# Performance work log

Hardware: AMD Instinct MI355X
Metric: run time of the kernel (lower is better)

Reference implementation:

```python
import jax, jax.numpy as jnp
import numpy as np

B, S, D, H = 2, 2048, 2048, 16
DK = D // H
EPS = 1e-5


def _layernorm(x, g, b):
    m = jnp.mean(x, axis=-1, keepdims=True)
    v = jnp.mean(jnp.square(x - m), axis=-1, keepdims=True)
    return (x - m) * jax.lax.rsqrt(v + EPS) * g + b


def setup_inputs() -> dict:
    key = jax.random.key(0)
    ks = jax.random.split(key, 12)
    w = lambda k, shape: jax.random.normal(k, shape, jnp.float32) * 0.02
    return {
        "src": jax.random.normal(ks[0], (B, S, D), jnp.float32),
        "src_mask": jnp.tril(jnp.ones((S, S), jnp.float32))[None, None],  # [1,1,S,S] causal
        "Wq": w(ks[1], (D, D)), "bq": jnp.zeros((D,), jnp.float32),
        "Wk": w(ks[2], (D, D)), "bk": jnp.zeros((D,), jnp.float32),
        "Wv": w(ks[3], (D, D)), "bv": jnp.zeros((D,), jnp.float32),
        "Wo": w(ks[4], (D, D)), "bo": jnp.zeros((D,), jnp.float32),
        "ln1_g": jnp.ones((D,), jnp.float32), "ln1_b": jnp.zeros((D,), jnp.float32),
        "ln2_g": jnp.ones((D,), jnp.float32), "ln2_b": jnp.zeros((D,), jnp.float32),
        "W1": w(ks[5], (D, 4 * D)), "b1": jnp.zeros((4 * D,), jnp.float32),
        "W2": w(ks[6], (4 * D, D)), "b2": jnp.zeros((D,), jnp.float32),
    }


def reference(src, src_mask, Wq, bq, Wk, bk, Wv, bv, Wo, bo,
              ln1_g, ln1_b, ln2_g, ln2_b, W1, b1, W2, b2):
    b, s, d = src.shape
    dk = d // H
    # --- pre-LN attention ---
    x = _layernorm(src, ln1_g, ln1_b)
    q = (x @ Wq + bq).reshape(b, s, H, dk).transpose(0, 2, 1, 3)  # [b,h,s,dk]
    k = (x @ Wk + bk).reshape(b, s, H, dk).transpose(0, 2, 1, 3)
    v = (x @ Wv + bv).reshape(b, s, H, dk).transpose(0, 2, 1, 3)
    scores = jnp.einsum('bhqd,bhkd->bhqk', q, k) / np.sqrt(dk).astype(np.float32)
    scores = jnp.where(src_mask > 0, scores, jnp.float32(-1e9))
    attn = jax.nn.softmax(scores, axis=-1)
    ctx = jnp.einsum('bhqk,bhkd->bhqd', attn, v)
    ctx = ctx.transpose(0, 2, 1, 3).reshape(b, s, d)
    x = src + (ctx @ Wo + bo)  # residual (dropout is identity at eval)
    # --- pre-LN MLP ---
    y = _layernorm(x, ln2_g, ln2_b)
    y = jax.nn.gelu(y @ W1 + b1, approximate=False) @ W2 + b2
    return x + y
```

## Files before the change

### kernel.cpp

```cpp
#include <hip/hip_runtime.h>
#include <hip/hip_bf16.h>
#include <math.h>

#define DEV __device__ __forceinline__

typedef __attribute__((ext_vector_type(8))) short short8;
typedef __attribute__((ext_vector_type(4))) float f32x4;

DEV short f2bf(float f) {
  union { float f; unsigned u; } v; v.f = f;
  unsigned r = v.u + 0x7fffu + ((v.u >> 16) & 1u);
  return (short)(r >> 16);
}

DEV void gload16(const void* g, void* l) {
  __builtin_amdgcn_global_load_lds(
      (__attribute__((address_space(1))) void*)g,
      (__attribute__((address_space(3))) void*)l, 16, 0, 0);
}

__global__ __launch_bounds__(256) void ln_kernel(
    const float* __restrict__ x, const float* __restrict__ g,
    const float* __restrict__ b, short* __restrict__ out) {
  int row = blockIdx.x;
  const float* xr = x + (size_t)row * 2048;
  int tid = threadIdx.x;
  float4 a0 = ((const float4*)xr)[tid * 2];
  float4 a1 = ((const float4*)xr)[tid * 2 + 1];
  float s = a0.x + a0.y + a0.z + a0.w + a1.x + a1.y + a1.z + a1.w;
  float q = a0.x*a0.x + a0.y*a0.y + a0.z*a0.z + a0.w*a0.w
          + a1.x*a1.x + a1.y*a1.y + a1.z*a1.z + a1.w*a1.w;
#pragma unroll
  for (int off = 32; off; off >>= 1) { s += __shfl_xor(s, off); q += __shfl_xor(q, off); }
  __shared__ float red[8];
  int w = tid >> 6;
  if ((tid & 63) == 0) { red[w] = s; red[4 + w] = q; }
  __syncthreads();
  s = red[0] + red[1] + red[2] + red[3];
  q = red[4] + red[5] + red[6] + red[7];
  float mean = s * (1.0f / 2048.0f);
  float var  = q * (1.0f / 2048.0f) - mean * mean;
  float rstd = rsqrtf(var + 1e-5f);
  float xv[8] = {a0.x, a0.y, a0.z, a0.w, a1.x, a1.y, a1.z, a1.w};
  short8 o;
#pragma unroll
  for (int j = 0; j < 8; ++j) {
    int col = tid * 8 + j;
    o[j] = f2bf((xv[j] - mean) * rstd * g[col] + b[col]);
  }
  *(short8*)(out + (size_t)row * 2048 + tid * 8) = o;
}

__global__ __launch_bounds__(256) void wt_kernel(
    const float* __restrict__ W, short* __restrict__ Wt, int K, int N) {
  __shared__ short tile[64][65];
  int k0 = blockIdx.x * 64, n0 = blockIdx.y * 64;
  int tx = threadIdx.x, ty = threadIdx.y;
#pragma unroll
  for (int r = 0; r < 16; ++r) {
    int kl = ty + r * 4;
    tile[kl][tx] = f2bf(W[(size_t)(k0 + kl) * N + n0 + tx]);
  }
  __syncthreads();
#pragma unroll
  for (int r = 0; r < 16; ++r) {
    int nl = ty + r * 4;
    Wt[(size_t)(n0 + nl) * K + k0 + tx] = tile[tx][nl];
  }
}

template <int EPI>
__global__ __launch_bounds__(256) void gemm_kernel(
    const short* __restrict__ A, const short* __restrict__ Bt, int K, int N,
    const float* __restrict__ bp1, const float* __restrict__ bp2,
    const float* __restrict__ bp3, const float* __restrict__ res,
    short* __restrict__ outb, float* __restrict__ outf, short* __restrict__ vt) {
  __shared__ char As[8192];
  __shared__ char Bs[8192];
  int tid = threadIdx.x, lane = tid & 63, w = tid >> 6;
  int wm = w >> 1, wn = w & 1;
  int hi = lane >> 4, lo = lane & 15;
  int bm = blockIdx.y * 128, bn = blockIdx.x * 128;

  int srow = 2 * w * 16 + (lane >> 2);
  int sslot = lane & 3;
  const short* Ag0 = A  + (size_t)(bm + srow) * K      + (sslot ^ (srow & 3)) * 8;
  const short* Ag1 = A  + (size_t)(bm + srow + 16) * K + (sslot ^ (srow & 3)) * 8;
  const short* Bg0 = Bt + (size_t)(bn + srow) * K      + (sslot ^ (srow & 3)) * 8;
  const short* Bg1 = Bt + (size_t)(bn + srow + 16) * K + (sslot ^ (srow & 3)) * 8;
  char* Al0 = As + 2 * w * 1024;  char* Al1 = Al0 + 1024;
  char* Bl0 = Bs + 2 * w * 1024;  char* Bl1 = Bl0 + 1024;

  const char* aRd[4]; const char* bRd[4];
#pragma unroll
  for (int i = 0; i < 4; ++i) {
    int ra = wm * 64 + i * 16 + lo;
    aRd[i] = As + ra * 64 + ((hi ^ (ra & 3)) << 4);
    int rb = wn * 64 + i * 16 + lo;
    bRd[i] = Bs + rb * 64 + ((hi ^ (rb & 3)) << 4);
  }

  f32x4 acc[4][4] = {};

  for (int k0 = 0; k0 < K; k0 += 32) {
    gload16(Ag0 + k0, Al0);
    gload16(Ag1 + k0, Al1);
    gload16(Bg0 + k0, Bl0);
    gload16(Bg1 + k0, Bl1);
    __syncthreads();
    short8 af[4], bf[4];
#pragma unroll
    for (int i = 0; i < 4; ++i) af[i] = *(const short8*)aRd[i];
#pragma unroll
    for (int i = 0; i < 4; ++i) bf[i] = *(const short8*)bRd[i];
#pragma unroll
    for (int mi = 0; mi < 4; ++mi)
#pragma unroll
      for (int ni = 0; ni < 4; ++ni)
        acc[mi][ni] = __builtin_amdgcn_mfma_f32_16x16x32_bf16(af[mi], bf[ni], acc[mi][ni], 0, 0, 0);
    __syncthreads();
  }

#pragma unroll
  for (int mi = 0; mi < 4; ++mi) {
#pragma unroll
    for (int ni = 0; ni < 4; ++ni) {
      int n = bn + wn * 64 + ni * 16 + lo;
#pragma unroll
      for (int r = 0; r < 4; ++r) {
        int m = bm + wm * 64 + mi * 16 + hi * 4 + r;
        float v = acc[mi][ni][r];
        if (EPI == 0) {
          float bb = (n < 2048) ? bp1[n] : (n < 4096) ? bp2[n - 2048] : bp3[n - 4096];
          v += bb;
          if (n < 2048) v *= 0.08838834764831845f;
          outb[(size_t)m * N + n] = f2bf(v);
          if (n >= 4096) {
            int b_ = m >> 11, s_ = m & 2047, h_ = (n - 4096) >> 7, dk = (n - 4096) & 127;
            vt[((size_t)((b_ * 16 + h_) * 128 + dk) << 11) + s_] = f2bf(v);
          }
        } else if (EPI == 1) {
          outf[(size_t)m * N + n] = res[(size_t)m * N + n] + v + bp1[n];
        } else {
          float t = v + bp1[n];
          outb[(size_t)m * N + n] = f2bf(0.5f * t * (1.0f + erff(t * 0.70710678118654752f)));
        }
      }
    }
  }
}

__global__ __launch_bounds__(256) void attn_kernel(
    const short* __restrict__ qkv, const short* __restrict__ vtb,
    short* __restrict__ ctx) {
  __shared__ char Kl[16384];
  __shared__ char Vl[16384];
  __shared__ char Pl[16384];
  int qt = blockIdx.x, bh = blockIdx.y;
  int b = bh >> 4, h = bh & 15;
  int tid = threadIdx.x, lane = tid & 63, w = tid >> 6;
  int hi = lane >> 4, lo = lane & 15;

  short8 qf[2][4];
#pragma unroll
  for (int mi = 0; mi < 2; ++mi)
#pragma unroll
    for (int ks = 0; ks < 4; ++ks) {
      int row = b * 2048 + qt * 128 + w * 32 + mi * 16 + lo;
      int col = h * 128 + ks * 32 + hi * 8;
      qf[mi][ks] = *(const short8*)(qkv + (size_t)row * 6144 + col);
    }

  f32x4 ao[2][8] = {};
  float mst[2][4], lst[2][4];
#pragma unroll
  for (int i = 0; i < 2; ++i)
#pragma unroll
    for (int r = 0; r < 4; ++r) { mst[i][r] = -1e30f; lst[i][r] = 0.f; }

  int nt = 2 * qt + 2;
  for (int t = 0; t < nt; ++t) {
    __syncthreads();
#pragma unroll
    for (int i = 0; i < 4; ++i) {
      int c = w * 4 + i;
      int kr = c * 4 + (lane >> 4);
      int dk16 = lo ^ (kr & 7);
      const short* kg = qkv + (size_t)(b * 2048 + t * 64 + kr) * 6144
                            + 2048 + h * 128 + dk16 * 8;
      gload16(kg, Kl + c * 1024);
      int vr = c * 8 + (lane >> 3);
      int kv16 = (lane & 7) ^ (vr & 7);
      const short* vg = vtb + (size_t)(bh * 128 + vr) * 2048 + t * 64 + kv16 * 8;
      gload16(vg, Vl + c * 1024);
    }
    __syncthreads();

    f32x4 sc[2][4] = {};
#pragma unroll
    for (int ks = 0; ks < 4; ++ks) {
      short8 kf[4];
#pragma unroll
      for (int ni = 0; ni < 4; ++ni) {
        int r = ni * 16 + lo;
        kf[ni] = *(const short8*)(Kl + r * 256 + (((ks * 4 + hi) ^ (r & 7)) << 4));
      }
#pragma unroll
      for (int mi = 0; mi < 2; ++mi)
#pragma unroll
        for (int ni = 0; ni < 4; ++ni)
          sc[mi][ni] = __builtin_amdgcn_mfma_f32_16x16x32_bf16(qf[mi][ks], kf[ni], sc[mi][ni], 0, 0, 0);
    }

    if (t >= 2 * qt) {
#pragma unroll
      for (int mi = 0; mi < 2; ++mi)
#pragma unroll
        for (int ni = 0; ni < 4; ++ni)
#pragma unroll
          for (int r = 0; r < 4; ++r) {
            int qrow = qt * 128 + w * 32 + mi * 16 + hi * 4 + r;
            int kv = t * 64 + ni * 16 + lo;
            if (kv > qrow) sc[mi][ni][r] = -1e9f;
          }
    }

#pragma unroll
    for (int mi = 0; mi < 2; ++mi)
#pragma unroll
      for (int r = 0; r < 4; ++r) {
        float vm = fmaxf(fmaxf(sc[mi][0][r], sc[mi][1][r]),
                         fmaxf(sc[mi][2][r], sc[mi][3][r]));
#pragma unroll
        for (int off = 8; off; off >>= 1) vm = fmaxf(vm, __shfl_xor(vm, off));
        float mn = fmaxf(mst[mi][r], vm);
        float corr = __expf(mst[mi][r] - mn);
        float ps = 0.f;
#pragma unroll
        for (int ni = 0; ni < 4; ++ni) {
          float p = __expf(sc[mi][ni][r] - mn);
          sc[mi][ni][r] = p; ps += p;
        }
#pragma unroll
        for (int off = 8; off; off >>= 1) ps += __shfl_xor(ps, off);
        lst[mi][r] = lst[mi][r] * corr + ps;
        mst[mi][r] = mn;
#pragma unroll
        for (int ni = 0; ni < 8; ++ni) ao[mi][ni][r] *= corr;
      }

#pragma unroll
    for (int mi = 0; mi < 2; ++mi)
#pragma unroll
      for (int ni = 0; ni < 4; ++ni)
#pragma unroll
        for (int r = 0; r < 4; ++r) {
          int rl = w * 32 + mi * 16 + hi * 4 + r;
          int byte = (rl * 128 + (ni * 16 + lo) * 2) ^ ((rl & 7) << 4);
          *(short*)(Pl + byte) = f2bf(sc[mi][ni][r]);
        }

#pragma unroll
    for (int ks = 0; ks < 2; ++ks) {
      short8 pf[2];
#pragma unroll
      for (int mi = 0; mi < 2; ++mi) {
        int r = w * 32 + mi * 16 + lo;
        pf[mi] = *(const short8*)(Pl + r * 128 + (((ks * 4 + hi) ^ (r & 7)) << 4));
      }
#pragma unroll
      for (int ni = 0; ni < 8; ++ni) {
        int r = ni * 16 + lo;
        short8 vf = *(const short8*)(Vl + r * 128 + (((ks * 4 + hi) ^ (r & 7)) << 4));
#pragma unroll
        for (int mi = 0; mi < 2; ++mi)
          ao[mi][ni] = __builtin_amdgcn_mfma_f32_16x16x32_bf16(pf[mi], vf, ao[mi][ni], 0, 0, 0);
      }
    }
  }

#pragma unroll
  for (int mi = 0; mi < 2; ++mi)
#pragma unroll
    for (int r = 0; r < 4; ++r) {
      float inv = 1.0f / lst[mi][r];
      int m = b * 2048 + qt * 128 + w * 32 + mi * 16 + hi * 4 + r;
#pragma unroll
      for (int ni = 0; ni < 8; ++ni) {
        int col = h * 128 + ni * 16 + lo;
        ctx[(size_t)m * 2048 + col] = f2bf(ao[mi][ni][r] * inv);
      }
    }
}

extern "C" void kernel_launch(void* const* d_in, const int* in_sizes, int n_in,
                              void* d_out, int out_size, void* d_ws, size_t ws_size,
                              hipStream_t stream) {
  const float* src = (const float*)d_in[0];
  const float* Wq = (const float*)d_in[2];  const float* bq = (const float*)d_in[3];
  const float* Wk = (const float*)d_in[4];  const float* bk = (const float*)d_in[5];
  const float* Wv = (const float*)d_in[6];  const float* bv = (const float*)d_in[7];
  const float* Wo = (const float*)d_in[8];  const float* bo = (const float*)d_in[9];
  const float* g1 = (const float*)d_in[10]; const float* be1 = (const float*)d_in[11];
  const float* g2 = (const float*)d_in[12]; const float* be2 = (const float*)d_in[13];
  const float* W1 = (const float*)d_in[14]; const float* b1 = (const float*)d_in[15];
  const float* W2 = (const float*)d_in[16]; const float* b2 = (const float*)d_in[17];

  char* ws = (char*)d_ws;
  short* x_ln = (short*)(ws);
  short* qkvb = (short*)(ws + 16777216);
  short* vtb  = (short*)(ws + 67108864);
  short* ctxb = (short*)(ws + 83886080);
  float* xbuf = (float*)(ws + 100663296);
  short* wt   = (short*)(ws + 134217728);
  short* hb   = (short*)(ws + 16777216);

  dim3 tb(64, 4);

  wt_kernel<<<dim3(32, 32), tb, 0, stream>>>(Wq, wt,                2048, 2048);
  wt_kernel<<<dim3(32, 32), tb, 0, stream>>>(Wk, wt + 2048 * 2048,  2048, 2048);
  wt_kernel<<<dim3(32, 32), tb, 0, stream>>>(Wv, wt + 4096 * 2048,  2048, 2048);
  ln_kernel<<<4096, 256, 0, stream>>>(src, g1, be1, x_ln);
  gemm_kernel<0><<<dim3(48, 32), 256, 0, stream>>>(
      x_ln, wt, 2048, 6144, bq, bk, bv, nullptr, qkvb, nullptr, vtb);
  attn_kernel<<<dim3(16, 32), 256, 0, stream>>>(qkvb, vtb, ctxb);
  wt_kernel<<<dim3(32, 32), tb, 0, stream>>>(Wo, wt, 2048, 2048);
  gemm_kernel<1><<<dim3(16, 32), 256, 0, stream>>>(
      ctxb, wt, 2048, 2048, bo, nullptr, nullptr, src, nullptr, xbuf, nullptr);
  ln_kernel<<<4096, 256, 0, stream>>>(xbuf, g2, be2, x_ln);
  wt_kernel<<<dim3(32, 128), tb, 0, stream>>>(W1, wt, 2048, 8192);
  gemm_kernel<2><<<dim3(64, 32), 256, 0, stream>>>(
      x_ln, wt, 2048, 8192, b1, nullptr, nullptr, nullptr, hb, nullptr, nullptr);
  wt_kernel<<<dim3(128, 32), tb, 0, stream>>>(W2, wt, 8192, 2048);
  gemm_kernel<1><<<dim3(16, 32), 256, 0, stream>>>(
      hb, wt, 8192, 2048, b2, nullptr, nullptr, xbuf, nullptr, (float*)d_out, nullptr);

  (void)in_sizes; (void)n_in; (void)out_size; (void)ws_size;
}
```

Measured before the change: 1.123 ms.

## Replace GEMM with 8-wave multi-buffered pipelined kernel using larger tiles

Replaces the single-buffered 128x128 four-wave GEMM with an eight-wave kernel that uses 256-wide N tiles (and 256 or 128 M tiles). It keeps four LDS stages, prefetches the next K-slices with global_load_lds while MFMAs run, and interleaves fine-grained barriers with setprio. The aim is to hide global memory latency, which the old loop exposed by syncing before every 32-wide K step, and to raise data reuse per block. In exchange it uses much more LDS, hand-written vmcnt waits that must match the load counts, and fewer blocks for the 2048-wide GEMMs.

New measurement: 985.7 us. 1.14x faster.

```diff
diff --git a/kernel.cpp b/kernel.cpp
--- a/kernel.cpp
+++ b/kernel.cpp
@@ -6,6 +6,8 @@
 
 typedef __attribute__((ext_vector_type(8))) short short8;
 typedef __attribute__((ext_vector_type(4))) float f32x4;
+
+template<bool B> struct BoolC { static constexpr bool value = B; };
 
 DEV short f2bf(float f) {
   union { float f; unsigned u; } v; v.f = f;
@@ -17,6 +19,17 @@
   __builtin_amdgcn_global_load_lds(
       (__attribute__((address_space(1))) void*)g,
       (__attribute__((address_space(3))) void*)l, 16, 0, 0);
+}
+
+DEV void bar() {
+  asm volatile("" ::: "memory");
+  __builtin_amdgcn_s_barrier();
+  asm volatile("" ::: "memory");
+}
+template<int N> DEV void vwait() {
+  if constexpr (N == 0)      asm volatile("s_waitcnt vmcnt(0)" ::: "memory");
+  else if constexpr (N == 3) asm volatile("s_waitcnt vmcnt(3)" ::: "memory");
+  else                       asm volatile("s_waitcnt vmcnt(4)" ::: "memory");
 }
 
 __global__ __launch_bounds__(256) void ln_kernel(
@@ -69,67 +82,140 @@
   }
 }
 
-template <int EPI>
-__global__ __launch_bounds__(256) void gemm_kernel(
+template <int BM, int EPI>
+__global__ __launch_bounds__(512, 2) void gemm8_kernel(
     const short* __restrict__ A, const short* __restrict__ Bt, int K, int N,
     const float* __restrict__ bp1, const float* __restrict__ bp2,
     const float* __restrict__ bp3, const float* __restrict__ res,
     short* __restrict__ outb, float* __restrict__ outf, short* __restrict__ vt) {
-  __shared__ char As[8192];
-  __shared__ char Bs[8192];
+  constexpr int MF  = BM / 32;
+  constexpr int MG  = MF / 2;
+  constexpr int SA  = BM * 64;
+  constexpr int SB  = 16384;
+  constexpr int CPA = BM / 128;
+  constexpr int CPB = 2;
+  constexpr int NW  = CPA + CPB;
+  __shared__ char lds[4 * SA + 4 * SB];
+  char* Ab = lds;
+  char* Bb = lds + 4 * SA;
   int tid = threadIdx.x, lane = tid & 63, w = tid >> 6;
-  int wm = w >> 1, wn = w & 1;
-  int hi = lane >> 4, lo = lane & 15;
-  int bm = blockIdx.y * 128, bn = blockIdx.x * 128;
-
-  int srow = 2 * w * 16 + (lane >> 2);
-  int sslot = lane & 3;
-  const short* Ag0 = A  + (size_t)(bm + srow) * K      + (sslot ^ (srow & 3)) * 8;
-  const short* Ag1 = A  + (size_t)(bm + srow + 16) * K + (sslot ^ (srow & 3)) * 8;
-  const short* Bg0 = Bt + (size_t)(bn + srow) * K      + (sslot ^ (srow & 3)) * 8;
-  const short* Bg1 = Bt + (size_t)(bn + srow + 16) * K + (sslot ^ (srow & 3)) * 8;
-  char* Al0 = As + 2 * w * 1024;  char* Al1 = Al0 + 1024;
-  char* Bl0 = Bs + 2 * w * 1024;  char* Bl1 = Bl0 + 1024;
-
-  const char* aRd[4]; const char* bRd[4];
-#pragma unroll
-  for (int i = 0; i < 4; ++i) {
-    int ra = wm * 64 + i * 16 + lo;
-    aRd[i] = As + ra * 64 + ((hi ^ (ra & 3)) << 4);
-    int rb = wn * 64 + i * 16 + lo;
-    bRd[i] = Bs + rb * 64 + ((hi ^ (rb & 3)) << 4);
-  }
-
-  f32x4 acc[4][4] = {};
-
-  for (int k0 = 0; k0 < K; k0 += 32) {
-    gload16(Ag0 + k0, Al0);
-    gload16(Ag1 + k0, Al1);
-    gload16(Bg0 + k0, Bl0);
-    gload16(Bg1 + k0, Bl1);
-    __syncthreads();
-    short8 af[4], bf[4];
-#pragma unroll
-    for (int i = 0; i < 4; ++i) af[i] = *(const short8*)aRd[i];
-#pragma unroll
-    for (int i = 0; i < 4; ++i) bf[i] = *(const short8*)bRd[i];
-#pragma unroll
-    for (int mi = 0; mi < 4; ++mi)
-#pragma unroll
-      for (int ni = 0; ni < 4; ++ni)
-        acc[mi][ni] = __builtin_amdgcn_mfma_f32_16x16x32_bf16(af[mi], bf[ni], acc[mi][ni], 0, 0, 0);
-    __syncthreads();
-  }
-
-#pragma unroll
-  for (int mi = 0; mi < 4; ++mi) {
-#pragma unroll
-    for (int ni = 0; ni < 4; ++ni) {
-      int n = bn + wn * 64 + ni * 16 + lo;
+  int wm = w >> 2, wn = w & 3, hi = lane >> 4, lo = lane & 15;
+  int bm = blockIdx.y * BM, bn = blockIdx.x * 256;
+
+  const char* gA[CPA]; int lA[CPA];
+  const char* gB[CPB]; int lB[CPB];
+#pragma unroll
+  for (int i = 0; i < CPA; ++i) {
+    int c = w * CPA + i, r = c * 16 + (lane >> 2);
+    gA[i] = (const char*)(A + (size_t)(bm + r) * K) + (((lane & 3) ^ ((r >> 1) & 3)) << 4);
+    lA[i] = c * 1024;
+  }
+#pragma unroll
+  for (int i = 0; i < CPB; ++i) {
+    int c = w * CPB + i, r = c * 16 + (lane >> 2);
+    gB[i] = (const char*)(Bt + (size_t)(bn + r) * K) + (((lane & 3) ^ ((r >> 1) & 3)) << 4);
+    lB[i] = c * 1024;
+  }
+  auto stA = [&](int g) {
+    char* d = Ab + (g & 3) * SA;
+#pragma unroll
+    for (int i = 0; i < CPA; ++i) gload16(gA[i] + (size_t)g * 64, d + lA[i]);
+  };
+  auto stB = [&](int g) {
+    char* d = Bb + (g & 3) * SB;
+#pragma unroll
+    for (int i = 0; i < CPB; ++i) gload16(gB[i] + (size_t)g * 64, d + lB[i]);
+  };
+
+  int offA[MF], offB[4];
+#pragma unroll
+  for (int m = 0; m < MF; ++m) {
+    int r = wm * (BM / 2) + m * 16 + lo;
+    offA[m] = r * 64 + ((hi ^ ((r >> 1) & 3)) << 4);
+  }
+#pragma unroll
+  for (int n = 0; n < 4; ++n) {
+    int r = wn * 64 + n * 16 + lo;
+    offB[n] = r * 64 + ((hi ^ ((r >> 1) & 3)) << 4);
+  }
+
+  f32x4 acc[MF][4];
+#pragma unroll
+  for (int m = 0; m < MF; ++m)
+#pragma unroll
+    for (int n = 0; n < 4; ++n) acc[m][n] = (f32x4){0.f, 0.f, 0.f, 0.f};
+
+  stA(0); stB(0); stA(1); stB(1);
+  vwait<NW>(); bar();
+
+  int NT = K >> 6;
+  auto tile = [&](int t, auto stc) {
+    constexpr bool ST = decltype(stc)::value;
+    char* sa0 = Ab + ((2 * t) & 3) * SA;     char* sb0 = Bb + ((2 * t) & 3) * SB;
+    char* sa1 = Ab + ((2 * t + 1) & 3) * SA; char* sb1 = Bb + ((2 * t + 1) & 3) * SB;
+    short8 bf[4], af[MG];
+#pragma unroll
+    for (int n = 0; n < 4; ++n) bf[n] = *(const short8*)(sb0 + offB[n]);
+#pragma unroll
+    for (int m = 0; m < MG; ++m) af[m] = *(const short8*)(sa0 + offA[m]);
+    if constexpr (ST) stA(2 * t + 2);
+    bar(); __builtin_amdgcn_s_setprio(1);
+#pragma unroll
+    for (int m = 0; m < MG; ++m)
+#pragma unroll
+      for (int n = 0; n < 4; ++n)
+        acc[m][n] = __builtin_amdgcn_mfma_f32_16x16x32_bf16(af[m], bf[n], acc[m][n], 0, 0, 0);
+    __builtin_amdgcn_s_setprio(0); bar();
+#pragma unroll
+    for (int m = 0; m < MG; ++m) af[m] = *(const short8*)(sa0 + offA[MG + m]);
+    if constexpr (ST) stB(2 * t + 2);
+    bar(); __builtin_amdgcn_s_setprio(1);
+#pragma unroll
+    for (int m = 0; m < MG; ++m)
+#pragma unroll
+      for (int n = 0; n < 4; ++n)
+        acc[MG + m][n] = __builtin_amdgcn_mfma_f32_16x16x32_bf16(af[m], bf[n], acc[MG + m][n], 0, 0, 0);
+    __builtin_amdgcn_s_setprio(0);
+    if constexpr (ST) vwait<NW>(); else vwait<0>();
+    bar();
+#pragma unroll
+    for (int n = 0; n < 4; ++n) bf[n] = *(const short8*)(sb1 + offB[n]);
+#pragma unroll
+    for (int m = 0; m < MG; ++m) af[m] = *(const short8*)(sa1 + offA[m]);
+    if constexpr (ST) stA(2 * t + 3);
+    bar(); __builtin_amdgcn_s_setprio(1);
+#pragma unroll
+    for (int m = 0; m < MG; ++m)
+#pragma unroll
+      for (int n = 0; n < 4; ++n)
+        acc[m][n] = __builtin_amdgcn_mfma_f32_16x16x32_bf16(af[m], bf[n], acc[m][n], 0, 0, 0);
+    __builtin_amdgcn_s_setprio(0); bar();
+#pragma unroll
+    for (int m = 0; m < MG; ++m) af[m] = *(const short8*)(sa1 + offA[MG + m]);
+    if constexpr (ST) stB(2 * t + 3);
+    bar(); __builtin_amdgcn_s_setprio(1);
+#pragma unroll
+    for (int m = 0; m < MG; ++m)
+#pragma unroll
+      for (int n = 0; n < 4; ++n)
+        acc[MG + m][n] = __builtin_amdgcn_mfma_f32_16x16x32_bf16(af[m], bf[n], acc[MG + m][n], 0, 0, 0);
+    __builtin_amdgcn_s_setprio(0);
+    if constexpr (ST) vwait<NW>();
+    bar();
+  };
+
+  for (int t = 0; t < NT - 1; ++t) tile(t, BoolC<true>{});
+  tile(NT - 1, BoolC<false>{});
+
+#pragma unroll
+  for (int mf = 0; mf < MF; ++mf) {
+#pragma unroll
+    for (int nf = 0; nf < 4; ++nf) {
+      int n = bn + wn * 64 + nf * 16 + lo;
 #pragma unroll
       for (int r = 0; r < 4; ++r) {
-        int m = bm + wm * 64 + mi * 16 + hi * 4 + r;
-        float v = acc[mi][ni][r];
+        int m = bm + wm * (BM / 2) + mf * 16 + hi * 4 + r;
+        float v = acc[mf][nf][r];
         if (EPI == 0) {
           float bb = (n < 2048) ? bp1[n] : (n < 4096) ? bp2[n - 2048] : bp3[n - 4096];
           v += bb;
@@ -321,18 +407,18 @@
   wt_kernel<<<dim3(32, 32), tb, 0, stream>>>(Wk, wt + 2048 * 2048,  2048, 2048);
   wt_kernel<<<dim3(32, 32), tb, 0, stream>>>(Wv, wt + 4096 * 2048,  2048, 2048);
   ln_kernel<<<4096, 256, 0, stream>>>(src, g1, be1, x_ln);
-  gemm_kernel<0><<<dim3(48, 32), 256, 0, stream>>>(
+  gemm8_kernel<256, 0><<<dim3(24, 16), 512, 0, stream>>>(
       x_ln, wt, 2048, 6144, bq, bk, bv, nullptr, qkvb, nullptr, vtb);
   attn_kernel<<<dim3(16, 32), 256, 0, stream>>>(qkvb, vtb, ctxb);
   wt_kernel<<<dim3(32, 32), tb, 0, stream>>>(Wo, wt, 2048, 2048);
-  gemm_kernel<1><<<dim3(16, 32), 256, 0, stream>>>(
+  gemm8_kernel<128, 1><<<dim3(8, 32), 512, 0, stream>>>(
       ctxb, wt, 2048, 2048, bo, nullptr, nullptr, src, nullptr, xbuf, nullptr);
   ln_kernel<<<4096, 256, 0, stream>>>(xbuf, g2, be2, x_ln);
   wt_kernel<<<dim3(32, 128), tb, 0, stream>>>(W1, wt, 2048, 8192);
-  gemm_kernel<2><<<dim3(64, 32), 256, 0, stream>>>(
+  gemm8_kernel<256, 2><<<dim3(32, 16), 512, 0, stream>>>(
       x_ln, wt, 2048, 8192, b1, nullptr, nullptr, nullptr, hb, nullptr, nullptr);
   wt_kernel<<<dim3(128, 32), tb, 0, stream>>>(W2, wt, 8192, 2048);
-  gemm_kernel<1><<<dim3(16, 32), 256, 0, stream>>>(
+  gemm8_kernel<128, 1><<<dim3(8, 32), 512, 0, stream>>>(
       hb, wt, 8192, 2048, b2, nullptr, nullptr, xbuf, nullptr, (float*)d_out, nullptr);
 
   (void)in_sizes; (void)n_in; (void)out_size; (void)ws_size;
```
